# Kernel optimization log

Measured on AMD Instinct MI355X. Metric: run time of the kernel, lower is better.

## Reference

```python
import jax, jax.numpy as jnp
import numpy as np

N_NODES = 100000
N_EDGES = 1600000
N_GRAPHS = 512
HIDDEN = 128
N_LAYERS = 3


def setup_inputs() -> dict:
    key = jax.random.key(0)
    ks = jax.random.split(key, 16)
    X = jax.random.normal(ks[0], (N_NODES, HIDDEN), dtype=jnp.float32)
    edge_index = jax.random.randint(ks[1], (2, N_EDGES), 0, N_NODES, dtype=jnp.int64)
    batch = jnp.sort(jax.random.randint(ks[2], (N_NODES,), 0, N_GRAPHS, dtype=jnp.int64))
    s = 1.0 / np.sqrt(HIDDEN)
    mlp_w1 = jax.random.normal(ks[3], (N_LAYERS, HIDDEN, HIDDEN), dtype=jnp.float32) * s
    mlp_b1 = jnp.zeros((N_LAYERS, HIDDEN), dtype=jnp.float32)
    mlp_w2 = jax.random.normal(ks[4], (N_LAYERS, HIDDEN, HIDDEN), dtype=jnp.float32) * s
    mlp_b2 = jnp.zeros((N_LAYERS, HIDDEN), dtype=jnp.float32)
    cls_w1 = jax.random.normal(ks[5], (HIDDEN * N_LAYERS, HIDDEN), dtype=jnp.float32) / np.sqrt(HIDDEN * N_LAYERS)
    cls_b1 = jnp.zeros((HIDDEN,), dtype=jnp.float32)
    cls_w2 = jax.random.normal(ks[6], (HIDDEN, HIDDEN), dtype=jnp.float32) * s
    cls_b2 = jnp.zeros((HIDDEN,), dtype=jnp.float32)
    cls_w3 = jax.random.normal(ks[7], (HIDDEN, 1), dtype=jnp.float32) * s
    cls_b3 = jnp.zeros((1,), dtype=jnp.float32)
    return {"X": X, "edge_index": edge_index, "batch": batch,
            "mlp_w1": mlp_w1, "mlp_b1": mlp_b1, "mlp_w2": mlp_w2, "mlp_b2": mlp_b2,
            "cls_w1": cls_w1, "cls_b1": cls_b1, "cls_w2": cls_w2, "cls_b2": cls_b2,
            "cls_w3": cls_w3, "cls_b3": cls_b3}


def reference(X, edge_index, batch, mlp_w1, mlp_b1, mlp_w2, mlp_b2,
              cls_w1, cls_b1, cls_w2, cls_b2, cls_w3, cls_b3):
    src, dst = edge_index[0], edge_index[1]
    xs = []
    for l in range(N_LAYERS):
        # GIN aggregation: sum_{j in N(i)} x_j ; eps = 0 so add self feature
        agg = jax.ops.segment_sum(X[src], dst, num_segments=N_NODES)  # [N, H]
        z = X + agg
        # 2-layer MLP update
        h = jax.nn.relu(z @ mlp_w1[l] + mlp_b1[l])
        h = h @ mlp_w2[l] + mlp_b2[l]
        # dropout is identity in eval; then relu
        X = jax.nn.relu(h)
        # global sum pooling per graph
        xs.append(jax.ops.segment_sum(X, batch, num_segments=N_GRAPHS))  # [G, H]
    h = jnp.concatenate(xs, axis=-1)  # JK 'cat' -> [G, H*L]
    h = jax.nn.relu(h @ cls_w1 + cls_b1)
    h = jax.nn.relu(h @ cls_w2 + cls_b2)
    logits = h @ cls_w3 + cls_b3  # [G, 1]
    return logits
```

## Files before the change

kernel.cpp:

```cpp
#include <hip/hip_runtime.h>
#include <hip/hip_fp16.h>
#include <cstddef>
#include <cstdint>

#define N_NODES   100000
#define N_EDGES   1600000
#define N_GRAPHS  512
#define HIDDEN    128
#define N_LAYERS  3

#define N_WIN        400
#define WIN_NODES    (N_NODES / N_WIN)
#define PLACE_BLOCKS 128
#define PCHUNK       (N_EDGES / PLACE_BLOCKS)

#define F2H_BLOCKS   ((N_NODES * HIDDEN / 8) / 256)
#define WCONV_BLOCKS (N_LAYERS * 2 * 16)
#define GB_BLOCKS    2
#define PREP_BLOCKS  (F2H_BLOCKS + WCONV_BLOCKS + GB_BLOCKS)

typedef _Float16 half8  __attribute__((ext_vector_type(8)));
typedef _Float16 half4v __attribute__((ext_vector_type(4)));
typedef _Float16 half2v __attribute__((ext_vector_type(2)));
typedef float    float8 __attribute__((ext_vector_type(8)));
typedef float    floatx4 __attribute__((ext_vector_type(4)));
typedef float    floatx2 __attribute__((ext_vector_type(2)));

__global__ __launch_bounds__(256) void win_count_kernel(const int* __restrict__ dst,
                                                        int* __restrict__ counts) {
    __shared__ int cs[N_WIN];
    for (int i = threadIdx.x; i < N_WIN; i += 256) cs[i] = 0;
    __syncthreads();
    const int4* d4 = (const int4*)(dst + blockIdx.x * PCHUNK);
    for (int i = threadIdx.x; i < PCHUNK / 4; i += 256) {
        int4 d = d4[i];
        atomicAdd(&cs[d.x / WIN_NODES], 1);
        atomicAdd(&cs[d.y / WIN_NODES], 1);
        atomicAdd(&cs[d.z / WIN_NODES], 1);
        atomicAdd(&cs[d.w / WIN_NODES], 1);
    }
    __syncthreads();
    for (int i = threadIdx.x; i < N_WIN; i += 256)
        counts[blockIdx.x * N_WIN + i] = cs[i];
}

__global__ __launch_bounds__(128) void win_scan1_kernel(const int* __restrict__ counts,
                                                        int* __restrict__ offsets,
                                                        int* __restrict__ colsum) {
    __shared__ int tmp[128];
    const int w = blockIdx.x;
    const int t = threadIdx.x;
    tmp[t] = counts[t * N_WIN + w];
    __syncthreads();
#pragma unroll
    for (int off = 1; off < 128; off <<= 1) {
        int u = (t >= off) ? tmp[t - off] : 0;
        __syncthreads();
        tmp[t] += u;
        __syncthreads();
    }
    offsets[t * N_WIN + w] = (t == 0) ? 0 : tmp[t - 1];
    if (t == 127) colsum[w] = tmp[127];
}

__global__ __launch_bounds__(512) void win_place_kernel(const int* __restrict__ src,
                                                        const int* __restrict__ dst,
                                                        const int* __restrict__ offsets,
                                                        const int* __restrict__ colsum,
                                                        int2* __restrict__ wedge) {
    __shared__ int ws[512];
    __shared__ int off[N_WIN];
    const int t = threadIdx.x;
    ws[t] = (t < N_WIN) ? colsum[t] : 0;
    __syncthreads();
#pragma unroll
    for (int o = 1; o < 512; o <<= 1) {
        int u = (t >= o) ? ws[t - o] : 0;
        __syncthreads();
        ws[t] += u;
        __syncthreads();
    }
    if (t < N_WIN) off[t] = offsets[blockIdx.x * N_WIN + t] + ((t == 0) ? 0 : ws[t - 1]);
    __syncthreads();
    const int4* d4 = (const int4*)(dst + blockIdx.x * PCHUNK);
    const int4* s4 = (const int4*)(src + blockIdx.x * PCHUNK);
    for (int i = t; i < PCHUNK / 4; i += 512) {
        int4 d = d4[i];
        int4 s = s4[i];
        int p0 = atomicAdd(&off[d.x / WIN_NODES], 1); wedge[p0] = make_int2(d.x, s.x);
        int p1 = atomicAdd(&off[d.y / WIN_NODES], 1); wedge[p1] = make_int2(d.y, s.y);
        int p2 = atomicAdd(&off[d.z / WIN_NODES], 1); wedge[p2] = make_int2(d.z, s.z);
        int p3 = atomicAdd(&off[d.w / WIN_NODES], 1); wedge[p3] = make_int2(d.w, s.w);
    }
}

__global__ __launch_bounds__(512) void win_csr_kernel(const int2* __restrict__ wedge,
                                                      const int* __restrict__ colsum,
                                                      int* __restrict__ row_ptr,
                                                      int* __restrict__ csr_src) {
    __shared__ int ws[512];
    __shared__ int cnt[WIN_NODES];
    __shared__ int bb[2];
    const int w = blockIdx.x, n0 = w * WIN_NODES, t = threadIdx.x;
    ws[t] = (t < N_WIN) ? colsum[t] : 0;
    __syncthreads();
#pragma unroll
    for (int o = 1; o < 512; o <<= 1) {
        int u = (t >= o) ? ws[t - o] : 0;
        __syncthreads();
        ws[t] += u;
        __syncthreads();
    }
    if (t == 0) { bb[0] = (w > 0) ? ws[w - 1] : 0; bb[1] = ws[w]; }
    if (w == N_WIN - 1 && t == 0) row_ptr[N_NODES] = ws[N_WIN - 1];
    for (int i = t; i < WIN_NODES; i += 512) cnt[i] = 0;
    __syncthreads();
    const int b0 = bb[0], b1 = bb[1];
    for (int e = b0 + t; e < b1; e += 512)
        atomicAdd(&cnt[wedge[e].x - n0], 1);
    __syncthreads();
    ws[t] = (t < WIN_NODES) ? cnt[t] : 0;
    __syncthreads();
#pragma unroll
    for (int o = 1; o < 512; o <<= 1) {
        int u = (t >= o) ? ws[t - o] : 0;
        __syncthreads();
        ws[t] += u;
        __syncthreads();
    }
    const int excl = (t == 0) ? 0 : ws[t - 1];
    if (t < WIN_NODES) {
        row_ptr[n0 + t] = b0 + excl;
        cnt[t] = b0 + excl;
    }
    __syncthreads();
    for (int e = b0 + t; e < b1; e += 512) {
        int2 ed = wedge[e];
        int p = atomicAdd(&cnt[ed.x - n0], 1);
        csr_src[p] = ed.y;
    }
}

__global__ __launch_bounds__(256) void prep_kernel(const float* __restrict__ X,
                                                   __half* __restrict__ hA,
                                                   unsigned char* __restrict__ outq,
                                                   const float* __restrict__ w1,
                                                   const float* __restrict__ w2,
                                                   __half* __restrict__ wt1,
                                                   __half* __restrict__ wt2,
                                                   const int* __restrict__ batch,
                                                   int* __restrict__ gstart) {
    __shared__ float tile[32][33];
    const int b = blockIdx.x;
    if (b < F2H_BLOCKS) {
        int t = b * 256 + threadIdx.x;
        const float4* in4 = (const float4*)X;
        float4 a = in4[t * 2 + 0];
        float4 c = in4[t * 2 + 1];
        __half2* o2 = (__half2*)hA;
        o2[t * 4 + 0] = __floats2half2_rn(a.x, a.y);
        o2[t * 4 + 1] = __floats2half2_rn(a.z, a.w);
        o2[t * 4 + 2] = __floats2half2_rn(c.x, c.y);
        o2[t * 4 + 3] = __floats2half2_rn(c.z, c.w);
        unsigned r0 = 0, r1 = 0;
        r0 = __builtin_amdgcn_cvt_pk_fp8_f32(a.x, a.y, r0, false);
        r0 = __builtin_amdgcn_cvt_pk_fp8_f32(a.z, a.w, r0, true);
        r1 = __builtin_amdgcn_cvt_pk_fp8_f32(c.x, c.y, r1, false);
        r1 = __builtin_amdgcn_cvt_pk_fp8_f32(c.z, c.w, r1, true);
        ((uint2*)outq)[t] = make_uint2(r0, r1);
    } else if (b < F2H_BLOCKS + WCONV_BLOCKS) {
        const int bb = b - F2H_BLOCKS;
        const int mat = bb & 1;
        const int tt = (bb >> 1) & 15;
        const int l  = bb >> 5;
        const int ti = (tt >> 2) * 32, tj = (tt & 3) * 32;
        const float* W = (mat ? w2 : w1) + (size_t)l * HIDDEN * HIDDEN;
        __half* WT = (mat ? wt2 : wt1) + (size_t)l * HIDDEN * HIDDEN;
        const int r = threadIdx.x >> 5;
        const int c = threadIdx.x & 31;
#pragma unroll
        for (int rr = 0; rr < 4; ++rr)
            tile[r + 8 * rr][c] = W[(size_t)(ti + r + 8 * rr) * HIDDEN + tj + c];
        __syncthreads();
#pragma unroll
        for (int rr = 0; rr < 4; ++rr)
            WT[(size_t)(tj + r + 8 * rr) * HIDDEN + ti + c] =
                __float2half(tile[c][r + 8 * rr]);
    } else {
        const int g = (b - F2H_BLOCKS - WCONV_BLOCKS) * 256 + threadIdx.x;
        if (g < N_GRAPHS) {
            int lo = 0, hi = N_NODES;
            while (lo < hi) {
                int mid = (lo + hi) >> 1;
                if (batch[mid] < g) lo = mid + 1; else hi = mid;
            }
            gstart[g] = lo;
        }
        if (g == 0) gstart[N_GRAPHS] = N_NODES;
    }
}

__device__ __forceinline__ void acc_fp8x16(float* acc, uint4 v) {
    floatx2 f;
    f = __builtin_amdgcn_cvt_pk_f32_fp8(v.x, false); acc[0] += f.x;  acc[1] += f.y;
    f = __builtin_amdgcn_cvt_pk_f32_fp8(v.x, true);  acc[2] += f.x;  acc[3] += f.y;
    f = __builtin_amdgcn_cvt_pk_f32_fp8(v.y, false); acc[4] += f.x;  acc[5] += f.y;
    f = __builtin_amdgcn_cvt_pk_f32_fp8(v.y, true);  acc[6] += f.x;  acc[7] += f.y;
    f = __builtin_amdgcn_cvt_pk_f32_fp8(v.z, false); acc[8] += f.x;  acc[9] += f.y;
    f = __builtin_amdgcn_cvt_pk_f32_fp8(v.z, true);  acc[10] += f.x; acc[11] += f.y;
    f = __builtin_amdgcn_cvt_pk_f32_fp8(v.w, false); acc[12] += f.x; acc[13] += f.y;
    f = __builtin_amdgcn_cvt_pk_f32_fp8(v.w, true);  acc[14] += f.x; acc[15] += f.y;
}

__device__ __forceinline__ void gather_body(int wave, int lane,
                                            const unsigned char* __restrict__ Xq,
                                            const __half* __restrict__ Xh,
                                            __half* __restrict__ Zh,
                                            const int* __restrict__ row_ptr,
                                            const int* __restrict__ csr_src) {
    const int grp = lane >> 3;
    const int m   = lane & 7;
    const uint4* Q = (const uint4*)Xq;

    float acc[16];
#pragma unroll
    for (int j = 0; j < 16; ++j) acc[j] = 0.f;

    int k = row_ptr[wave];
    const int end = row_ptr[wave + 1];

    for (; k + 16 <= end; k += 16) {
        int n0 = csr_src[k + grp];
        int n1 = csr_src[k + 8 + grp];
        uint4 v0 = Q[(size_t)n0 * 8 + m];
        uint4 v1 = Q[(size_t)n1 * 8 + m];
        acc_fp8x16(acc, v0);
        acc_fp8x16(acc, v1);
    }
    if (k + 8 <= end) {
        int n0 = csr_src[k + grp];
        uint4 v0 = Q[(size_t)n0 * 8 + m];
        acc_fp8x16(acc, v0);
        k += 8;
    }
    int rem = end - k;
    if (grp < rem) {
        int n0 = csr_src[k + grp];
        uint4 v0 = Q[(size_t)n0 * 8 + m];
        acc_fp8x16(acc, v0);
    }

    half2v hh[8];
#pragma unroll
    for (int j = 0; j < 8; ++j) {
        hh[j][0] = (_Float16)acc[2 * j];
        hh[j][1] = (_Float16)acc[2 * j + 1];
    }
#pragma unroll
    for (int j = 0; j < 8; ++j) {
        int b = __shfl_xor(__builtin_bit_cast(int, hh[j]), 8);
        hh[j] = hh[j] + __builtin_bit_cast(half2v, b);
    }
#pragma unroll
    for (int j = 0; j < 8; ++j) {
        int b = __shfl_xor(__builtin_bit_cast(int, hh[j]), 16);
        hh[j] = hh[j] + __builtin_bit_cast(half2v, b);
    }
#pragma unroll
    for (int j = 0; j < 8; ++j) {
        int b = __shfl_xor(__builtin_bit_cast(int, hh[j]), 32);
        hh[j] = hh[j] + __builtin_bit_cast(half2v, b);
    }

    if (grp == 0) {
        const half2v* H2 = (const half2v*)(Xh + (size_t)wave * HIDDEN + 16 * m);
        half8 o0, o1;
#pragma unroll
        for (int j = 0; j < 4; ++j) {
            half2v s = hh[j] + H2[j];
            o0[2 * j] = s[0]; o0[2 * j + 1] = s[1];
        }
#pragma unroll
        for (int j = 0; j < 4; ++j) {
            half2v s = hh[4 + j] + H2[4 + j];
            o1[2 * j] = s[0]; o1[2 * j + 1] = s[1];
        }
        ((half8*)(Zh + (size_t)wave * HIDDEN + 16 * m))[0] = o0;
        ((half8*)(Zh + (size_t)wave * HIDDEN + 16 * m))[1] = o1;
    }
}

__global__ void gather_kernel(const unsigned char* __restrict__ Xq,
                              const __half* __restrict__ Xh,
                              __half* __restrict__ Zh,
                              const int* __restrict__ row_ptr,
                              const int* __restrict__ csr_src) {
    int wave = (blockIdx.x * blockDim.x + threadIdx.x) >> 6;
    if (wave >= N_NODES) return;
    gather_body(wave, threadIdx.x & 63, Xq, Xh, Zh, row_ptr, csr_src);
}

__device__ __forceinline__ void gpool_body(int g,
                                           const __half* __restrict__ Xh,
                                           const int* __restrict__ gstart,
                                           float* __restrict__ pooled, int layer) {
    __shared__ float red[16][16][8];
    const int f8 = threadIdx.x & 15;
    const int qt = threadIdx.x >> 4;
    const int s = gstart[g], e = gstart[g + 1];

    float acc[8];
#pragma unroll
    for (int j = 0; j < 8; ++j) acc[j] = 0.f;

    for (int n = s + qt; n < e; n += 16) {
        half8 v = ((const half8*)(Xh + (size_t)n * HIDDEN))[f8];
#pragma unroll
        for (int j = 0; j < 8; ++j) acc[j] += (float)v[j];
    }
#pragma unroll
    for (int j = 0; j < 8; ++j) red[qt][f8][j] = acc[j];
    __syncthreads();

    if (threadIdx.x < 128) {
        const int c = threadIdx.x;
        float sum = 0.f;
#pragma unroll
        for (int p = 0; p < 16; ++p) sum += red[p][c >> 3][c & 7];
        pooled[(size_t)g * (HIDDEN * N_LAYERS) + layer * HIDDEN + c] = sum;
    }
}

__global__ __launch_bounds__(256) void gpool_kernel(const __half* __restrict__ Xh,
                                                    const int* __restrict__ gstart,
                                                    float* __restrict__ pooled,
                                                    int layer) {
    gpool_body(blockIdx.x, Xh, gstart, pooled, layer);
}

#define POOL_BLKS N_GRAPHS
__global__ __launch_bounds__(256) void gather_pool_kernel(const unsigned char* __restrict__ Xq,
                                                          const __half* __restrict__ Xh,
                                                          __half* __restrict__ Zh,
                                                          const int* __restrict__ row_ptr,
                                                          const int* __restrict__ csr_src,
                                                          const int* __restrict__ gstart,
                                                          float* __restrict__ pooled,
                                                          int prev_layer) {
    if (blockIdx.x < POOL_BLKS) {
        gpool_body(blockIdx.x, Xh, gstart, pooled, prev_layer);
        return;
    }
    int wave = ((blockIdx.x - POOL_BLKS) * 256 + threadIdx.x) >> 6;
    if (wave >= N_NODES) return;
    gather_body(wave, threadIdx.x & 63, Xq, Xh, Zh, row_ptr, csr_src);
}

#define MMF_BLOCKS 512
__global__ __launch_bounds__(512, 4) void mlp_ws_kernel(const __half* __restrict__ A,
                                                        const __half* __restrict__ Wt1,
                                                        const __half* __restrict__ Wt2,
                                                        const float* __restrict__ b1,
                                                        const float* __restrict__ b2,
                                                        __half* __restrict__ C16,
                                                        unsigned char* __restrict__ Q8) {
    __shared__ _Float16 hs[2][16][128];

    const int tid  = threadIdx.x;
    const int wv   = tid >> 6;
    const int lane = tid & 63;
    const int m    = lane & 15;
    const int q    = lane >> 4;
    const int NTILES = N_NODES / 16;

    half8 wf1[4], wf2[4];
    float bl1[4], bl2[4];
    {
        const half8* W1row = (const half8*)(Wt1 + (size_t)(wv * 16 + m) * HIDDEN);
        const half8* W2row = (const half8*)(Wt2 + (size_t)(wv * 16 + m) * HIDDEN);
#pragma unroll
        for (int c = 0; c < 4; ++c) { wf1[c] = W1row[c * 4 + q]; wf2[c] = W2row[c * 4 + q]; }
#pragma unroll
        for (int r = 0; r < 4; ++r) {
            bl1[r] = b1[wv * 16 + q * 4 + r];
            bl2[r] = b2[wv * 16 + q * 4 + r];
        }
    }

    _Float16* hwr0 = &hs[0][m][(((2 * wv + (q >> 1)) ^ m) << 3) + ((q & 1) << 2)];
    _Float16* hwr1 = &hs[1][m][(((2 * wv + (q >> 1)) ^ m) << 3) + ((q & 1) << 2)];
    const _Float16* hrd0 = &hs[0][m][0];
    const _Float16* hrd1 = &hs[1][m][0];

    int t = blockIdx.x;
    half8 c0, c1, c2, c3, p0, p1, p2, p3;
    {
        const half8* Ar = (const half8*)(A + (size_t)(t * 16 + m) * HIDDEN);
        c0 = Ar[q]; c1 = Ar[4 + q]; c2 = Ar[8 + q]; c3 = Ar[12 + q];
    }
    if (t + MMF_BLOCKS < NTILES) {
        const half8* Ar = (const half8*)(A + (size_t)((t + MMF_BLOCKS) * 16 + m) * HIDDEN);
        p0 = Ar[q]; p1 = Ar[4 + q]; p2 = Ar[8 + q]; p3 = Ar[12 + q];
    }

    int buf = 0;
    while (true) {
        const int t2 = t + 2 * MMF_BLOCKS;
        half8 f0, f1, f2, f3;
        if (t2 < NTILES) {
            const half8* Ar = (const half8*)(A + (size_t)(t2 * 16 + m) * HIDDEN);
            f0 = Ar[q]; f1 = Ar[4 + q]; f2 = Ar[8 + q]; f3 = Ar[12 + q];
        }

        {
            floatx4 acc = {0.f, 0.f, 0.f, 0.f};
            acc = __builtin_amdgcn_mfma_f32_16x16x32_f16(wf1[0], c0, acc, 0, 0, 0);
            acc = __builtin_amdgcn_mfma_f32_16x16x32_f16(wf1[1], c1, acc, 0, 0, 0);
            acc = __builtin_amdgcn_mfma_f32_16x16x32_f16(wf1[2], c2, acc, 0, 0, 0);
            acc = __builtin_amdgcn_mfma_f32_16x16x32_f16(wf1[3], c3, acc, 0, 0, 0);
            half4v o;
#pragma unroll
            for (int r = 0; r < 4; ++r) o[r] = (_Float16)fmaxf(acc[r] + bl1[r], 0.f);
            *(half4v*)(buf ? hwr1 : hwr0) = o;
        }
        __builtin_amdgcn_sched_barrier(0);
        asm volatile("s_waitcnt lgkmcnt(0)" ::: "memory");
        __builtin_amdgcn_s_barrier();
        __builtin_amdgcn_sched_barrier(0);

        {
            const _Float16* hr = buf ? hrd1 : hrd0;
            half8 h0 = *(const half8*)(hr + (((0 + q) ^ m) << 3));
            half8 h1 = *(const half8*)(hr + (((4 + q) ^ m) << 3));
            half8 h2 = *(const half8*)(hr + (((8 + q) ^ m) << 3));
            half8 h3 = *(const half8*)(hr + (((12 + q) ^ m) << 3));
            floatx4 acc = {0.f, 0.f, 0.f, 0.f};
            acc = __builtin_amdgcn_mfma_f32_16x16x32_f16(wf2[0], h0, acc, 0, 0, 0);
            acc = __builtin_amdgcn_mfma_f32_16x16x32_f16(wf2[1], h1, acc, 0, 0, 0);
            acc = __builtin_amdgcn_mfma_f32_16x16x32_f16(wf2[2], h2, acc, 0, 0, 0);
            acc = __builtin_amdgcn_mfma_f32_16x16x32_f16(wf2[3], h3, acc, 0, 0, 0);
            float v0 = fmaxf(acc[0] + bl2[0], 0.f);
            float v1 = fmaxf(acc[1] + bl2[1], 0.f);
            float v2 = fmaxf(acc[2] + bl2[2], 0.f);
            float v3 = fmaxf(acc[3] + bl2[3], 0.f);
            const size_t base = (size_t)(t * 16 + m) * HIDDEN + wv * 16 + q * 4;
            half4v o;
            o[0] = (_Float16)v0; o[1] = (_Float16)v1;
            o[2] = (_Float16)v2; o[3] = (_Float16)v3;
            *(half4v*)(C16 + base) = o;
            if (Q8) {
                unsigned r0 = 0;
                r0 = __builtin_amdgcn_cvt_pk_fp8_f32(v0, v1, r0, false);
                r0 = __builtin_amdgcn_cvt_pk_fp8_f32(v2, v3, r0, true);
                *(unsigned*)(Q8 + base) = r0;
            }
        }

        if (t + MMF_BLOCKS >= NTILES) break;
        t += MMF_BLOCKS;
        c0 = p0; c1 = p1; c2 = p2; c3 = p3;
        p0 = f0; p1 = f1; p2 = f2; p3 = f3;
        buf ^= 1;
    }
}

__global__ __launch_bounds__(128) void cls_kernel(const float* __restrict__ pooled,
                                                  const float* __restrict__ w1,
                                                  const float* __restrict__ b1,
                                                  const float* __restrict__ w2,
                                                  const float* __restrict__ b2,
                                                  const float* __restrict__ w3,
                                                  const float* __restrict__ b3,
                                                  float* __restrict__ out) {
    __shared__ float hin[HIDDEN * N_LAYERS];
    __shared__ float h1[HIDDEN];
    __shared__ float red[HIDDEN];
    const int g = blockIdx.x;
    const int t = threadIdx.x;

    for (int i = t; i < HIDDEN * N_LAYERS; i += 128)
        hin[i] = pooled[(size_t)g * (HIDDEN * N_LAYERS) + i];
    __syncthreads();

    float s = 0.f;
    for (int k = 0; k < HIDDEN * N_LAYERS; ++k) s += hin[k] * w1[(size_t)k * HIDDEN + t];
    s = fmaxf(s + b1[t], 0.f);
    h1[t] = s;
    __syncthreads();

    float s2 = 0.f;
    for (int k = 0; k < HIDDEN; ++k) s2 += h1[k] * w2[(size_t)k * HIDDEN + t];
    s2 = fmaxf(s2 + b2[t], 0.f);

    red[t] = s2 * w3[t];
    __syncthreads();
    for (int off = 64; off > 0; off >>= 1) {
        if (t < off) red[t] += red[t + off];
        __syncthreads();
    }
    if (t == 0) out[g] = red[0] + b3[0];
}

extern "C" void kernel_launch(void* const* d_in, const int* in_sizes, int n_in,
                              void* d_out, int out_size, void* d_ws, size_t ws_size,
                              hipStream_t stream) {
    const float* X     = (const float*)d_in[0];
    const int*   ei    = (const int*)d_in[1];
    const int*   batch = (const int*)d_in[2];
    const float* w1all = (const float*)d_in[3];
    const float* b1all = (const float*)d_in[4];
    const float* w2all = (const float*)d_in[5];
    const float* b2all = (const float*)d_in[6];
    const float* cw1   = (const float*)d_in[7];
    const float* cb1   = (const float*)d_in[8];
    const float* cw2   = (const float*)d_in[9];
    const float* cb2   = (const float*)d_in[10];
    const float* cw3   = (const float*)d_in[11];
    const float* cb3   = (const float*)d_in[12];
    float* out = (float*)d_out;

    const int* src = ei;
    const int* dst = ei + N_EDGES;

    char* p = (char*)d_ws;
    auto alloc2 = [&](size_t bytes) {
        char* r = p;
        p += (bytes + 255) & ~(size_t)255;
        return r;
    };
    __half* hA      = (__half*)alloc2((size_t)N_NODES * HIDDEN * sizeof(__half));
    __half* hB      = (__half*)alloc2((size_t)N_NODES * HIDDEN * sizeof(__half));
    __half* zh      = (__half*)alloc2((size_t)N_NODES * HIDDEN * sizeof(__half));
    unsigned char* qbuf = (unsigned char*)alloc2((size_t)N_NODES * HIDDEN);
    __half* wt1     = (__half*)alloc2((size_t)N_LAYERS * HIDDEN * HIDDEN * sizeof(__half));
    __half* wt2     = (__half*)alloc2((size_t)N_LAYERS * HIDDEN * HIDDEN * sizeof(__half));
    int2*   wedge   = (int2*)alloc2((size_t)N_EDGES * sizeof(int2));
    int*    csr     = (int*)alloc2((size_t)N_EDGES * sizeof(int));
    int*    rowp    = (int*)alloc2((size_t)(N_NODES + 1) * sizeof(int));
    int*    counts  = (int*)alloc2((size_t)PLACE_BLOCKS * N_WIN * sizeof(int));
    int*    offsets = (int*)alloc2((size_t)PLACE_BLOCKS * N_WIN * sizeof(int));
    int*    colsum  = (int*)alloc2((size_t)N_WIN * sizeof(int));
    int*    gstart  = (int*)alloc2((size_t)(N_GRAPHS + 1) * sizeof(int));
    float*  pooled  = (float*)alloc2((size_t)N_GRAPHS * HIDDEN * N_LAYERS * sizeof(float));

    win_count_kernel<<<PLACE_BLOCKS, 256, 0, stream>>>(dst, counts);
    win_scan1_kernel<<<N_WIN, 128, 0, stream>>>(counts, offsets, colsum);
    win_place_kernel<<<PLACE_BLOCKS, 512, 0, stream>>>(src, dst, offsets, colsum, wedge);
    win_csr_kernel<<<N_WIN, 512, 0, stream>>>(wedge, colsum, rowp, csr);

    prep_kernel<<<PREP_BLOCKS, 256, 0, stream>>>(X, hA, qbuf, w1all, w2all, wt1, wt2,
                                                 batch, gstart);

    const int gat_grid = (N_NODES + 3) / 4;

    __half* hcur = hA;
    for (int l = 0; l < N_LAYERS; ++l) {
        __half* hnext = (l & 1) ? hA : hB;
        const bool emit = (l < N_LAYERS - 1);
        if (l == 0) {
            gather_kernel<<<gat_grid, 256, 0, stream>>>(qbuf, hcur, zh, rowp, csr);
        } else {
            gather_pool_kernel<<<gat_grid + POOL_BLKS, 256, 0, stream>>>(
                qbuf, hcur, zh, rowp, csr, gstart, pooled, l - 1);
        }
        mlp_ws_kernel<<<MMF_BLOCKS, 512, 0, stream>>>(zh,
                                                      wt1 + (size_t)l * HIDDEN * HIDDEN,
                                                      wt2 + (size_t)l * HIDDEN * HIDDEN,
                                                      b1all + (size_t)l * HIDDEN,
                                                      b2all + (size_t)l * HIDDEN,
                                                      hnext,
                                                      emit ? qbuf : (unsigned char*)nullptr);
        hcur = hnext;
    }

    gpool_kernel<<<N_GRAPHS, 256, 0, stream>>>(hcur, gstart, pooled, N_LAYERS - 1);
    cls_kernel<<<N_GRAPHS, 128, 0, stream>>>(pooled, cw1, cb1, cw2, cb2, cw3, cb3, out);
}
```

Before: 436.7 us.

## Fuse edge counting into prep kernel, drop scan kernel, merge final pool with classifier

Merges the window-count pass into the prep kernel as extra blocks and removes the separate per-window scan kernel. Each place block now computes its own column prefix from a transposed counts array. The final-layer graph pooling is fused with the classifier MLP into one kernel. The goal is to cut three kernel launches and the sync gaps between them. In exchange, every place block redundantly reads 128 counts per window, and the classifier now runs in the same 256-thread blocks as the pooling.

```diff
diff --git a/kernel.cpp b/kernel.cpp
--- a/kernel.cpp
+++ b/kernel.cpp
@@ -17,7 +17,7 @@
 #define F2H_BLOCKS   ((N_NODES * HIDDEN / 8) / 256)
 #define WCONV_BLOCKS (N_LAYERS * 2 * 16)
 #define GB_BLOCKS    2
-#define PREP_BLOCKS  (F2H_BLOCKS + WCONV_BLOCKS + GB_BLOCKS)
+#define PREPC_BLOCKS (PLACE_BLOCKS + F2H_BLOCKS + WCONV_BLOCKS + GB_BLOCKS)
 
 typedef _Float16 half8  __attribute__((ext_vector_type(8)));
 typedef _Float16 half4v __attribute__((ext_vector_type(4)));
@@ -26,134 +26,36 @@
 typedef float    floatx4 __attribute__((ext_vector_type(4)));
 typedef float    floatx2 __attribute__((ext_vector_type(2)));
 
-__global__ __launch_bounds__(256) void win_count_kernel(const int* __restrict__ dst,
-                                                        int* __restrict__ counts) {
-    __shared__ int cs[N_WIN];
-    for (int i = threadIdx.x; i < N_WIN; i += 256) cs[i] = 0;
-    __syncthreads();
-    const int4* d4 = (const int4*)(dst + blockIdx.x * PCHUNK);
-    for (int i = threadIdx.x; i < PCHUNK / 4; i += 256) {
-        int4 d = d4[i];
-        atomicAdd(&cs[d.x / WIN_NODES], 1);
-        atomicAdd(&cs[d.y / WIN_NODES], 1);
-        atomicAdd(&cs[d.z / WIN_NODES], 1);
-        atomicAdd(&cs[d.w / WIN_NODES], 1);
-    }
-    __syncthreads();
-    for (int i = threadIdx.x; i < N_WIN; i += 256)
-        counts[blockIdx.x * N_WIN + i] = cs[i];
-}
-
-__global__ __launch_bounds__(128) void win_scan1_kernel(const int* __restrict__ counts,
-                                                        int* __restrict__ offsets,
-                                                        int* __restrict__ colsum) {
-    __shared__ int tmp[128];
-    const int w = blockIdx.x;
-    const int t = threadIdx.x;
-    tmp[t] = counts[t * N_WIN + w];
-    __syncthreads();
-#pragma unroll
-    for (int off = 1; off < 128; off <<= 1) {
-        int u = (t >= off) ? tmp[t - off] : 0;
-        __syncthreads();
-        tmp[t] += u;
-        __syncthreads();
-    }
-    offsets[t * N_WIN + w] = (t == 0) ? 0 : tmp[t - 1];
-    if (t == 127) colsum[w] = tmp[127];
-}
-
-__global__ __launch_bounds__(512) void win_place_kernel(const int* __restrict__ src,
-                                                        const int* __restrict__ dst,
-                                                        const int* __restrict__ offsets,
-                                                        const int* __restrict__ colsum,
-                                                        int2* __restrict__ wedge) {
-    __shared__ int ws[512];
-    __shared__ int off[N_WIN];
-    const int t = threadIdx.x;
-    ws[t] = (t < N_WIN) ? colsum[t] : 0;
-    __syncthreads();
-#pragma unroll
-    for (int o = 1; o < 512; o <<= 1) {
-        int u = (t >= o) ? ws[t - o] : 0;
-        __syncthreads();
-        ws[t] += u;
-        __syncthreads();
-    }
-    if (t < N_WIN) off[t] = offsets[blockIdx.x * N_WIN + t] + ((t == 0) ? 0 : ws[t - 1]);
-    __syncthreads();
-    const int4* d4 = (const int4*)(dst + blockIdx.x * PCHUNK);
-    const int4* s4 = (const int4*)(src + blockIdx.x * PCHUNK);
-    for (int i = t; i < PCHUNK / 4; i += 512) {
-        int4 d = d4[i];
-        int4 s = s4[i];
-        int p0 = atomicAdd(&off[d.x / WIN_NODES], 1); wedge[p0] = make_int2(d.x, s.x);
-        int p1 = atomicAdd(&off[d.y / WIN_NODES], 1); wedge[p1] = make_int2(d.y, s.y);
-        int p2 = atomicAdd(&off[d.z / WIN_NODES], 1); wedge[p2] = make_int2(d.z, s.z);
-        int p3 = atomicAdd(&off[d.w / WIN_NODES], 1); wedge[p3] = make_int2(d.w, s.w);
-    }
-}
-
-__global__ __launch_bounds__(512) void win_csr_kernel(const int2* __restrict__ wedge,
-                                                      const int* __restrict__ colsum,
-                                                      int* __restrict__ row_ptr,
-                                                      int* __restrict__ csr_src) {
-    __shared__ int ws[512];
-    __shared__ int cnt[WIN_NODES];
-    __shared__ int bb[2];
-    const int w = blockIdx.x, n0 = w * WIN_NODES, t = threadIdx.x;
-    ws[t] = (t < N_WIN) ? colsum[t] : 0;
-    __syncthreads();
-#pragma unroll
-    for (int o = 1; o < 512; o <<= 1) {
-        int u = (t >= o) ? ws[t - o] : 0;
-        __syncthreads();
-        ws[t] += u;
-        __syncthreads();
-    }
-    if (t == 0) { bb[0] = (w > 0) ? ws[w - 1] : 0; bb[1] = ws[w]; }
-    if (w == N_WIN - 1 && t == 0) row_ptr[N_NODES] = ws[N_WIN - 1];
-    for (int i = t; i < WIN_NODES; i += 512) cnt[i] = 0;
-    __syncthreads();
-    const int b0 = bb[0], b1 = bb[1];
-    for (int e = b0 + t; e < b1; e += 512)
-        atomicAdd(&cnt[wedge[e].x - n0], 1);
-    __syncthreads();
-    ws[t] = (t < WIN_NODES) ? cnt[t] : 0;
-    __syncthreads();
-#pragma unroll
-    for (int o = 1; o < 512; o <<= 1) {
-        int u = (t >= o) ? ws[t - o] : 0;
-        __syncthreads();
-        ws[t] += u;
-        __syncthreads();
-    }
-    const int excl = (t == 0) ? 0 : ws[t - 1];
-    if (t < WIN_NODES) {
-        row_ptr[n0 + t] = b0 + excl;
-        cnt[t] = b0 + excl;
-    }
-    __syncthreads();
-    for (int e = b0 + t; e < b1; e += 512) {
-        int2 ed = wedge[e];
-        int p = atomicAdd(&cnt[ed.x - n0], 1);
-        csr_src[p] = ed.y;
-    }
-}
-
-__global__ __launch_bounds__(256) void prep_kernel(const float* __restrict__ X,
-                                                   __half* __restrict__ hA,
-                                                   unsigned char* __restrict__ outq,
-                                                   const float* __restrict__ w1,
-                                                   const float* __restrict__ w2,
-                                                   __half* __restrict__ wt1,
-                                                   __half* __restrict__ wt2,
-                                                   const int* __restrict__ batch,
-                                                   int* __restrict__ gstart) {
+__global__ __launch_bounds__(256) void prep_count_kernel(const float* __restrict__ X,
+                                                         __half* __restrict__ hA,
+                                                         unsigned char* __restrict__ outq,
+                                                         const float* __restrict__ w1,
+                                                         const float* __restrict__ w2,
+                                                         __half* __restrict__ wt1,
+                                                         __half* __restrict__ wt2,
+                                                         const int* __restrict__ batch,
+                                                         int* __restrict__ gstart,
+                                                         const int* __restrict__ dst,
+                                                         int* __restrict__ counts) {
     __shared__ float tile[32][33];
+    __shared__ int   cs[N_WIN];
     const int b = blockIdx.x;
-    if (b < F2H_BLOCKS) {
-        int t = b * 256 + threadIdx.x;
+    if (b < PLACE_BLOCKS) {
+        for (int i = threadIdx.x; i < N_WIN; i += 256) cs[i] = 0;
+        __syncthreads();
+        const int4* d4 = (const int4*)(dst + b * PCHUNK);
+        for (int i = threadIdx.x; i < PCHUNK / 4; i += 256) {
+            int4 d = d4[i];
+            atomicAdd(&cs[d.x / WIN_NODES], 1);
+            atomicAdd(&cs[d.y / WIN_NODES], 1);
+            atomicAdd(&cs[d.z / WIN_NODES], 1);
+            atomicAdd(&cs[d.w / WIN_NODES], 1);
+        }
+        __syncthreads();
+        for (int i = threadIdx.x; i < N_WIN; i += 256)
+            counts[i * PLACE_BLOCKS + b] = cs[i];
+    } else if (b < PLACE_BLOCKS + F2H_BLOCKS) {
+        int t = (b - PLACE_BLOCKS) * 256 + threadIdx.x;
         const float4* in4 = (const float4*)X;
         float4 a = in4[t * 2 + 0];
         float4 c = in4[t * 2 + 1];
@@ -168,8 +70,8 @@
         r1 = __builtin_amdgcn_cvt_pk_fp8_f32(c.x, c.y, r1, false);
         r1 = __builtin_amdgcn_cvt_pk_fp8_f32(c.z, c.w, r1, true);
         ((uint2*)outq)[t] = make_uint2(r0, r1);
-    } else if (b < F2H_BLOCKS + WCONV_BLOCKS) {
-        const int bb = b - F2H_BLOCKS;
+    } else if (b < PLACE_BLOCKS + F2H_BLOCKS + WCONV_BLOCKS) {
+        const int bb = b - PLACE_BLOCKS - F2H_BLOCKS;
         const int mat = bb & 1;
         const int tt = (bb >> 1) & 15;
         const int l  = bb >> 5;
@@ -187,7 +89,7 @@
             WT[(size_t)(tj + r + 8 * rr) * HIDDEN + ti + c] =
                 __float2half(tile[c][r + 8 * rr]);
     } else {
-        const int g = (b - F2H_BLOCKS - WCONV_BLOCKS) * 256 + threadIdx.x;
+        const int g = (b - PLACE_BLOCKS - F2H_BLOCKS - WCONV_BLOCKS) * 256 + threadIdx.x;
         if (g < N_GRAPHS) {
             int lo = 0, hi = N_NODES;
             while (lo < hi) {
@@ -197,6 +99,97 @@
             gstart[g] = lo;
         }
         if (g == 0) gstart[N_GRAPHS] = N_NODES;
+    }
+}
+
+__global__ __launch_bounds__(512) void win_place_kernel(const int* __restrict__ src,
+                                                        const int* __restrict__ dst,
+                                                        const int* __restrict__ counts,
+                                                        int* __restrict__ colsum,
+                                                        int2* __restrict__ wedge) {
+    __shared__ int ws[512];
+    __shared__ int off[N_WIN];
+    const int t = threadIdx.x;
+    const int b = blockIdx.x;
+
+    int total = 0, part = 0;
+    if (t < N_WIN) {
+        const int* col = counts + t * PLACE_BLOCKS;
+#pragma unroll 4
+        for (int bb = 0; bb < PLACE_BLOCKS; ++bb) {
+            int v = col[bb];
+            total += v;
+            if (bb < b) part += v;
+        }
+        if (b == 0) colsum[t] = total;
+    }
+    ws[t] = (t < N_WIN) ? total : 0;
+    __syncthreads();
+#pragma unroll
+    for (int o = 1; o < 512; o <<= 1) {
+        int u = (t >= o) ? ws[t - o] : 0;
+        __syncthreads();
+        ws[t] += u;
+        __syncthreads();
+    }
+    if (t < N_WIN) off[t] = part + ((t == 0) ? 0 : ws[t - 1]);
+    __syncthreads();
+    const int4* d4 = (const int4*)(dst + b * PCHUNK);
+    const int4* s4 = (const int4*)(src + b * PCHUNK);
+    for (int i = t; i < PCHUNK / 4; i += 512) {
+        int4 d = d4[i];
+        int4 s = s4[i];
+        int p0 = atomicAdd(&off[d.x / WIN_NODES], 1); wedge[p0] = make_int2(d.x, s.x);
+        int p1 = atomicAdd(&off[d.y / WIN_NODES], 1); wedge[p1] = make_int2(d.y, s.y);
+        int p2 = atomicAdd(&off[d.z / WIN_NODES], 1); wedge[p2] = make_int2(d.z, s.z);
+        int p3 = atomicAdd(&off[d.w / WIN_NODES], 1); wedge[p3] = make_int2(d.w, s.w);
+    }
+}
+
+__global__ __launch_bounds__(512) void win_csr_kernel(const int2* __restrict__ wedge,
+                                                      const int* __restrict__ colsum,
+                                                      int* __restrict__ row_ptr,
+                                                      int* __restrict__ csr_src) {
+    __shared__ int ws[512];
+    __shared__ int cnt[WIN_NODES];
+    __shared__ int bb[2];
+    const int w = blockIdx.x, n0 = w * WIN_NODES, t = threadIdx.x;
+    ws[t] = (t < N_WIN) ? colsum[t] : 0;
+    __syncthreads();
+#pragma unroll
+    for (int o = 1; o < 512; o <<= 1) {
+        int u = (t >= o) ? ws[t - o] : 0;
+        __syncthreads();
+        ws[t] += u;
+        __syncthreads();
+    }
+    if (t == 0) { bb[0] = (w > 0) ? ws[w - 1] : 0; bb[1] = ws[w]; }
+    if (w == N_WIN - 1 && t == 0) row_ptr[N_NODES] = ws[N_WIN - 1];
+    for (int i = t; i < WIN_NODES; i += 512) cnt[i] = 0;
+    __syncthreads();
+    const int b0 = bb[0], b1 = bb[1];
+    for (int e = b0 + t; e < b1; e += 512)
+        atomicAdd(&cnt[wedge[e].x - n0], 1);
+    __syncthreads();
+    ws[t] = (t < WIN_NODES) ? cnt[t] : 0;
+    __syncthreads();
+#pragma unroll
+    for (int o = 1; o < 512; o <<= 1) {
+        int u = (t >= o) ? ws[t - o] : 0;
+        __syncthreads();
+        ws[t] += u;
+        __syncthreads();
+    }
+    const int excl = (t == 0) ? 0 : ws[t - 1];
+    if (t < WIN_NODES) {
+        row_ptr[n0 + t] = b0 + excl;
+        cnt[t] = b0 + excl;
+    }
+    __syncthreads();
+    for (int e = b0 + t; e < b1; e += 512) {
+        int2 ed = wedge[e];
+        int p = atomicAdd(&cnt[ed.x - n0], 1);
+        csr_src[p] = ed.y;
     }
 }
 
@@ -329,13 +322,6 @@
         for (int p = 0; p < 16; ++p) sum += red[p][c >> 3][c & 7];
         pooled[(size_t)g * (HIDDEN * N_LAYERS) + layer * HIDDEN + c] = sum;
     }
-}
-
-__global__ __launch_bounds__(256) void gpool_kernel(const __half* __restrict__ Xh,
-                                                    const int* __restrict__ gstart,
-                                                    float* __restrict__ pooled,
-                                                    int layer) {
-    gpool_body(blockIdx.x, Xh, gstart, pooled, layer);
 }
 
 #define POOL_BLKS N_GRAPHS
@@ -354,6 +340,69 @@
     int wave = ((blockIdx.x - POOL_BLKS) * 256 + threadIdx.x) >> 6;
     if (wave >= N_NODES) return;
     gather_body(wave, threadIdx.x & 63, Xq, Xh, Zh, row_ptr, csr_src);
+}
+
+__global__ __launch_bounds__(256) void gpool_cls_kernel(const __half* __restrict__ Xh,
+                                                        const int* __restrict__ gstart,
+                                                        const float* __restrict__ pooled,
+                                                        const float* __restrict__ w1,
+                                                        const float* __restrict__ b1,
+                                                        const float* __restrict__ w2,
+                                                        const float* __restrict__ b2,
+                                                        const float* __restrict__ w3,
+                                                        const float* __restrict__ b3,
+                                                        float* __restrict__ out) {
+    __shared__ float red[16][16][8];
+    __shared__ float hin[HIDDEN * N_LAYERS];
+    __shared__ float h1v[HIDDEN];
+    __shared__ float redc[HIDDEN];
+    const int g   = blockIdx.x;
+    const int tid = threadIdx.x;
+    const int f8  = tid & 15;
+    const int qt  = tid >> 4;
+    const int s = gstart[g], e = gstart[g + 1];
+
+    for (int i = tid; i < 2 * HIDDEN; i += 256)
+        hin[i] = pooled[(size_t)g * (HIDDEN * N_LAYERS) + i];
+
+    float acc[8];
+#pragma unroll
+    for (int j = 0; j < 8; ++j) acc[j] = 0.f;
+    for (int n = s + qt; n < e; n += 16) {
+        half8 v = ((const half8*)(Xh + (size_t)n * HIDDEN))[f8];
+#pragma unroll
+        for (int j = 0; j < 8; ++j) acc[j] += (float)v[j];
+    }
+#pragma unroll
+    for (int j = 0; j < 8; ++j) red[qt][f8][j] = acc[j];
+    __syncthreads();
+    if (tid < 128) {
+        float sum = 0.f;
+#pragma unroll
+        for (int p = 0; p < 16; ++p) sum += red[p][tid >> 3][tid & 7];
+        hin[2 * HIDDEN + tid] = sum;
+    }
+    __syncthreads();
+
+    if (tid < 128) {
+        float sacc = 0.f;
+        for (int k = 0; k < HIDDEN * N_LAYERS; ++k)
+            sacc += hin[k] * w1[(size_t)k * HIDDEN + tid];
+        h1v[tid] = fmaxf(sacc + b1[tid], 0.f);
+    }
+    __syncthreads();
+    if (tid < 128) {
+        float s2 = 0.f;
+        for (int k = 0; k < HIDDEN; ++k) s2 += h1v[k] * w2[(size_t)k * HIDDEN + tid];
+        s2 = fmaxf(s2 + b2[tid], 0.f);
+        redc[tid] = s2 * w3[tid];
+    }
+    __syncthreads();
+    for (int off = 64; off > 0; off >>= 1) {
+        if (tid < off) redc[tid] += redc[tid + off];
+        __syncthreads();
+    }
+    if (tid == 0) out[g] = redc[0] + b3[0];
 }
 
 #define MMF_BLOCKS 512
@@ -464,43 +513,6 @@
     }
 }
 
-__global__ __launch_bounds__(128) void cls_kernel(const float* __restrict__ pooled,
-                                                  const float* __restrict__ w1,
-                                                  const float* __restrict__ b1,
-                                                  const float* __restrict__ w2,
-                                                  const float* __restrict__ b2,
-                                                  const float* __restrict__ w3,
-                                                  const float* __restrict__ b3,
-                                                  float* __restrict__ out) {
-    __shared__ float hin[HIDDEN * N_LAYERS];
-    __shared__ float h1[HIDDEN];
-    __shared__ float red[HIDDEN];
-    const int g = blockIdx.x;
-    const int t = threadIdx.x;
-
-    for (int i = t; i < HIDDEN * N_LAYERS; i += 128)
-        hin[i] = pooled[(size_t)g * (HIDDEN * N_LAYERS) + i];
-    __syncthreads();
-
-    float s = 0.f;
-    for (int k = 0; k < HIDDEN * N_LAYERS; ++k) s += hin[k] * w1[(size_t)k * HIDDEN + t];
-    s = fmaxf(s + b1[t], 0.f);
-    h1[t] = s;
-    __syncthreads();
-
-    float s2 = 0.f;
-    for (int k = 0; k < HIDDEN; ++k) s2 += h1[k] * w2[(size_t)k * HIDDEN + t];
-    s2 = fmaxf(s2 + b2[t], 0.f);
-
-    red[t] = s2 * w3[t];
-    __syncthreads();
-    for (int off = 64; off > 0; off >>= 1) {
-        if (t < off) red[t] += red[t + off];
-        __syncthreads();
-    }
-    if (t == 0) out[g] = red[0] + b3[0];
-}
-
 extern "C" void kernel_launch(void* const* d_in, const int* in_sizes, int n_in,
                               void* d_out, int out_size, void* d_ws, size_t ws_size,
                               hipStream_t stream) {
@@ -538,18 +550,15 @@
     int*    csr     = (int*)alloc2((size_t)N_EDGES * sizeof(int));
     int*    rowp    = (int*)alloc2((size_t)(N_NODES + 1) * sizeof(int));
     int*    counts  = (int*)alloc2((size_t)PLACE_BLOCKS * N_WIN * sizeof(int));
-    int*    offsets = (int*)alloc2((size_t)PLACE_BLOCKS * N_WIN * sizeof(int));
     int*    colsum  = (int*)alloc2((size_t)N_WIN * sizeof(int));
     int*    gstart  = (int*)alloc2((size_t)(N_GRAPHS + 1) * sizeof(int));
     float*  pooled  = (float*)alloc2((size_t)N_GRAPHS * HIDDEN * N_LAYERS * sizeof(float));
 
-    win_count_kernel<<<PLACE_BLOCKS, 256, 0, stream>>>(dst, counts);
-    win_scan1_kernel<<<N_WIN, 128, 0, stream>>>(counts, offsets, colsum);
-    win_place_kernel<<<PLACE_BLOCKS, 512, 0, stream>>>(src, dst, offsets, colsum, wedge);
+    prep_count_kernel<<<PREPC_BLOCKS, 256, 0, stream>>>(X, hA, qbuf, w1all, w2all,
+                                                        wt1, wt2, batch, gstart,
+                                                        dst, counts);
+    win_place_kernel<<<PLACE_BLOCKS, 512, 0, stream>>>(src, dst, counts, colsum, wedge);
     win_csr_kernel<<<N_WIN, 512, 0, stream>>>(wedge, colsum, rowp, csr);
-
-    prep_kernel<<<PREP_BLOCKS, 256, 0, stream>>>(X, hA, qbuf, w1all, w2all, wt1, wt2,
-                                                 batch, gstart);
 
     const int gat_grid = (N_NODES + 3) / 4;
 
@@ -573,6 +582,6 @@
         hcur = hnext;
     }
 
-    gpool_kernel<<<N_GRAPHS, 256, 0, stream>>>(hcur, gstart, pooled, N_LAYERS - 1);
-    cls_kernel<<<N_GRAPHS, 128, 0, stream>>>(pooled, cw1, cb1, cw2, cb2, cw3, cb3, out);
-}
+    gpool_cls_kernel<<<N_GRAPHS, 256, 0, stream>>>(hcur, gstart, pooled,
+                                                   cw1, cb1, cw2, cb2, cw3, cb3, out);
+}
```

New measurement: 436.8 us. Within noise of the previous version (+0.0%).
